# Kernel tuning notes

Hardware: AMD Instinct MI355X
Metric: run time of the kernel (lower is better)

## Reference

```python
import jax, jax.numpy as jnp
import numpy as np

EPS = 1e-5
K_SIZE, STRIDE, DILATION, N_HEADS = 8, 2, 2, 8


def ln2d(x, w, b):
    # LayerNorm2d: normalize over channel axis of NCHW
    m = x.mean(1, keepdims=True)
    v = x.var(1, keepdims=True)
    return (x - m) * jax.lax.rsqrt(v + EPS) * w[None, :, None, None] + b[None, :, None, None]


def setup_inputs() -> dict:
    key = jax.random.key(0)
    ks = jax.random.split(key, 8)
    B, C, H, W = 1, 64, 128, 128
    hid = 2 * C  # ffn_ratio = 2
    f = lambda k, s: jax.random.normal(k, s, jnp.float32) * 0.02
    return dict(
        x=jax.random.normal(ks[0], (B, C, H, W), jnp.float32),
        norm1_w=jnp.ones(C, jnp.float32), norm1_b=jnp.zeros(C, jnp.float32),
        qkv_w=f(ks[1], (3 * C, C)), qkv_b=jnp.zeros(3 * C, jnp.float32),
        qn_w=jnp.ones(C, jnp.float32), qn_b=jnp.zeros(C, jnp.float32),
        kn_w=jnp.ones(C, jnp.float32), kn_b=jnp.zeros(C, jnp.float32),
        proj_w=f(ks[2], (C, C)), proj_b=jnp.zeros(C, jnp.float32),
        gamma1=jnp.full((C,), 0.1, jnp.float32),
        norm2_w=jnp.ones(C, jnp.float32), norm2_b=jnp.zeros(C, jnp.float32),
        fc1_w=f(ks[3], (hid, C)), fc1_b=jnp.zeros(hid, jnp.float32),
        mn_w=jnp.ones(hid, jnp.float32), mn_b=jnp.zeros(hid, jnp.float32),
        fc2_w=f(ks[4], (C, hid)), fc2_b=jnp.zeros(C, jnp.float32),
        gamma2=jnp.full((C,), 0.1, jnp.float32),
    )


def reference(x, norm1_w, norm1_b, qkv_w, qkv_b, qn_w, qn_b, kn_w, kn_b,
              proj_w, proj_b, gamma1, norm2_w, norm2_b,
              fc1_w, fc1_b, mn_w, mn_b, fc2_w, fc2_b, gamma2):
    B, C, H, W = x.shape
    n = N_HEADS
    hd = C // n
    # strided + dilated neighborhood offsets (includes 0 at center)
    off = (jnp.arange(K_SIZE) * STRIDE - (K_SIZE * STRIDE) // 2) * DILATION

    # ---- neighborhood attention branch ----
    xn = ln2d(x, norm1_w, norm1_b)
    qkv = jnp.einsum('oc,bchw->bohw', qkv_w, xn) + qkv_b[None, :, None, None]
    q, k, v = jnp.split(qkv, 3, axis=1)
    q = ln2d(q, qn_w, qn_b)
    k = ln2d(k, kn_w, kn_b)
    q = q.reshape(B, n, hd, H, W)
    k = k.reshape(B, n, hd, H, W)
    v = v.reshape(B, n, hd, H, W)

    pos_h = jnp.arange(H)[:, None] + off[None, :]            # [H, k]
    vh = (pos_h >= 0) & (pos_h < H)
    ih = jnp.clip(pos_h, 0, H - 1)
    pos_w = jnp.arange(W)[:, None] + off[None, :]            # [W, k]
    vw = (pos_w >= 0) & (pos_w < W)
    iw = jnp.clip(pos_w, 0, W - 1)

    # gather neighborhoods: [B,n,hd,H,kh,W,kw]
    Kg = jnp.take(jnp.take(k, ih, axis=3), iw, axis=5)
    Vg = jnp.take(jnp.take(v, ih, axis=3), iw, axis=5)

    scores = jnp.einsum('bnchw,bnchiwj->bnhwij', q, Kg) * (hd ** -0.5)
    mask = vh[:, None, :, None] & vw[None, :, None, :]        # [H,W,kh,kw]
    scores = jnp.where(mask[None, None], scores, -jnp.inf)
    a = jax.nn.softmax(scores.reshape(B, n, H, W, -1), axis=-1).reshape(scores.shape)
    o = jnp.einsum('bnhwij,bnchiwj->bnchw', a, Vg).reshape(B, C, H, W)
    o = jnp.einsum('oc,bchw->bohw', proj_w, o) + proj_b[None, :, None, None]
    x = x + gamma1[None, :, None, None] * o                  # ls1 + residual (drop_path=0)

    # ---- ConvMlp branch: 1x1 conv -> norm -> silu -> 1x1 conv ----
    y = ln2d(x, norm2_w, norm2_b)
    h1 = jnp.einsum('oc,bchw->bohw', fc1_w, y) + fc1_b[None, :, None, None]
    h1 = jax.nn.silu(ln2d(h1, mn_w, mn_b))
    h2 = jnp.einsum('oc,bchw->bohw', fc2_w, h1) + fc2_b[None, :, None, None]
    return x + gamma2[None, :, None, None] * h2
```

## Files before the change

### kernel.cpp

```cpp
#include <hip/hip_runtime.h>
#include <math.h>

#define HW 16384
#define CC 64
#define HID 128
#define EPSV 1e-5f
#define ROW 36
#define SROW 69
#define HDSTR 131072


__global__ __launch_bounds__(256) void k_ln_qkv(
    const float* __restrict__ x,
    const float* __restrict__ n1w, const float* __restrict__ n1b,
    const float* __restrict__ qkvw, const float* __restrict__ qkvb,
    const float* __restrict__ qnw, const float* __restrict__ qnb,
    const float* __restrict__ knw, const float* __restrict__ knb,
    float* __restrict__ qo, float* __restrict__ ko, float* __restrict__ vo)
{
    __shared__ __align__(16) float xs[CC][ROW];
    __shared__ __align__(16) float qk[32][SROW];
    __shared__ __align__(16) float mu1[32], rs1[32], mu2[32], rs2[32];

    const int t = threadIdx.x;
    const int pix0 = blockIdx.x * 32;
    const int sel = blockIdx.y;

    {
        const int c = t >> 2, pxq = (t & 3) * 8;
        *(float4*)&xs[c][pxq]     = *(const float4*)(x + c * HW + pix0 + pxq);
        *(float4*)&xs[c][pxq + 4] = *(const float4*)(x + c * HW + pix0 + pxq + 4);
    }
    __syncthreads();

    if (t < 128) {
        const int px = ((t >> 6) << 4) + (t & 15);
        const int part = (t & 63) >> 4;
        float s = 0.f, ss = 0.f;
        #pragma unroll
        for (int i = 0; i < 16; ++i) { float v = xs[part * 16 + i][px]; s += v; ss += v * v; }
        s += __shfl_xor(s, 16); ss += __shfl_xor(ss, 16);
        s += __shfl_xor(s, 32); ss += __shfl_xor(ss, 32);
        if (part == 0) {
            float m = s * (1.f / CC);
            mu1[px] = m;
            rs1[px] = rsqrtf(ss * (1.f / CC) - m * m + EPSV);
        }
    }
    __syncthreads();

    {
        const int c = t >> 2, pxq = (t & 3) * 8;
        const float wgt = n1w[c], bia = n1b[c];
        #pragma unroll
        for (int hh = 0; hh < 2; ++hh) {
            float4 v = *(float4*)&xs[c][pxq + hh * 4];
            float4 m4 = *(float4*)&mu1[pxq + hh * 4];
            float4 r4 = *(float4*)&rs1[pxq + hh * 4];
            v.x = (v.x - m4.x) * r4.x * wgt + bia;
            v.y = (v.y - m4.y) * r4.y * wgt + bia;
            v.z = (v.z - m4.z) * r4.z * wgt + bia;
            v.w = (v.w - m4.w) * r4.w * wgt + bia;
            *(float4*)&xs[c][pxq + hh * 4] = v;
        }
    }
    __syncthreads();

    {
        const int o0 = (t >> 3) * 2;
        const int px0 = (t & 7) * 4;
        const int ow = sel * 64 + o0;
        float a[2][4];
        #pragma unroll
        for (int j = 0; j < 2; ++j) {
            float b = qkvb[ow + j];
            a[j][0] = b; a[j][1] = b; a[j][2] = b; a[j][3] = b;
        }
        for (int c = 0; c < CC; c += 4) {
            float4 xv[4];
            #pragma unroll
            for (int i = 0; i < 4; ++i) xv[i] = *(float4*)&xs[c + i][px0];
            #pragma unroll
            for (int j = 0; j < 2; ++j) {
                float4 wv = *(const float4*)(qkvw + (ow + j) * CC + c);
                #pragma unroll
                for (int pp = 0; pp < 4; ++pp) {
                    a[j][pp] += wv.x * (&xv[0].x)[pp] + wv.y * (&xv[1].x)[pp]
                              + wv.z * (&xv[2].x)[pp] + wv.w * (&xv[3].x)[pp];
                }
            }
        }
        #pragma unroll
        for (int j = 0; j < 2; ++j) {
            #pragma unroll
            for (int pp = 0; pp < 4; ++pp) qk[px0 + pp][o0 + j] = a[j][pp];
        }
    }
    __syncthreads();

    if (sel < 2) {
        if (t < 128) {
            const int px = ((t >> 6) << 4) + (t & 15);
            const int part = (t & 63) >> 4;
            float s = 0.f, ss = 0.f;
            #pragma unroll
            for (int i = 0; i < 16; ++i) { float v = qk[px][part * 16 + i]; s += v; ss += v * v; }
            s += __shfl_xor(s, 16); ss += __shfl_xor(ss, 16);
            s += __shfl_xor(s, 32); ss += __shfl_xor(ss, 32);
            if (part == 0) {
                float m = s * (1.f / CC);
                mu2[px] = m;
                rs2[px] = rsqrtf(ss * (1.f / CC) - m * m + EPSV);
            }
        }
        __syncthreads();
    }

    const float* lw = (sel == 0) ? qnw : knw;
    const float* lb = (sel == 0) ? qnb : knb;
    float* dst = (sel == 0) ? qo : ((sel == 1) ? ko : vo);
    #pragma unroll
    for (int pass = 0; pass < 2; ++pass) {
        const int px = (t >> 4) + pass * 16;
        const int cg = t & 15;
        const int c = cg * 4;
        const int hd = cg >> 1;
        const int d4 = (cg & 1) * 4;
        const int pixel = pix0 + px;
        const int h = pixel >> 7, w = pixel & 127;
        const int pos = ((h >> 2) * 32 + (w >> 2)) * 16 + (h & 3) * 4 + (w & 3);
        const int gbase = hd * HDSTR + pos * 8 + d4;

        float4 vv = *(float4*)&qk[px][c];
        if (sel < 2) {
            const float mm = mu2[px], rr = rs2[px];
            float4 w4 = *(const float4*)(lw + c);
            float4 b4 = *(const float4*)(lb + c);
            vv.x = (vv.x - mm) * rr * w4.x + b4.x;
            vv.y = (vv.y - mm) * rr * w4.y + b4.y;
            vv.z = (vv.z - mm) * rr * w4.z + b4.z;
            vv.w = (vv.w - mm) * rr * w4.w + b4.w;
        }
        *(float4*)(dst + gbase) = vv;
    }
}

__global__ __launch_bounds__(256) void k_attn(
    const float* __restrict__ q, const float* __restrict__ k, const float* __restrict__ v,
    float* __restrict__ o)
{
    __shared__ __align__(16) float kt[4][15][33][2];
    __shared__ __align__(16) float vt[4][15][33][2];

    const int t = threadIdx.x;
    const int band = blockIdx.x;
    const int sub  = blockIdx.y;
    const int head = blockIdx.z;
    const int hs0 = band * 8;

    const float* kb = k + head * HDSTR;
    const float* vb = v + head * HDSTR;

    for (int idx = t; idx < 960; idx += 256) {
        const int row = idx >> 6;
        const int rem = idx & 63;
        const int ws = rem >> 1;
        const int dh = rem & 1;
        int gr = hs0 - 4 + row;
        gr = gr < 0 ? 0 : (gr > 31 ? 31 : gr);
        const int gaddr = ((gr * 32 + ws) * 16 + sub) * 8 + dh * 4;
        const float4 kv4 = *(const float4*)(kb + gaddr);
        const float4 vv4 = *(const float4*)(vb + gaddr);
        const int dp = dh * 2;
        kt[dp][row][ws][0] = kv4.x;     kt[dp][row][ws][1] = kv4.y;
        kt[dp + 1][row][ws][0] = kv4.z; kt[dp + 1][row][ws][1] = kv4.w;
        vt[dp][row][ws][0] = vv4.x;     vt[dp][row][ws][1] = vv4.y;
        vt[dp + 1][row][ws][0] = vv4.z; vt[dp + 1][row][ws][1] = vv4.w;
    }

    const int r = t >> 5;
    const int ws = t & 31;
    const int hs = hs0 + r;

    const float* qp = q + head * HDSTR + ((hs * 32 + ws) * 16 + sub) * 8;
    const float4 q0 = *(const float4*)qp;
    const float4 q1 = *(const float4*)(qp + 4);
    const float scale = 0.35355339059327373f;

    __syncthreads();

    float s[64];
    float mx0 = -1e30f, mx1 = -1e30f, mx2 = -1e30f, mx3 = -1e30f;
    #pragma unroll
    for (int i = 0; i < 8; ++i) {
        const int lr = r + i;
        const bool vh = (unsigned)(hs + i - 4) < 32u;
        #pragma unroll
        for (int j = 0; j < 8; ++j) {
            const int cs = ws + j - 4;
            const bool valid = vh && ((unsigned)cs < 32u);
            const int cc = cs < 0 ? 0 : (cs > 31 ? 31 : cs);
            const float2 kA = *(const float2*)&kt[0][lr][cc][0];
            const float2 kB = *(const float2*)&kt[1][lr][cc][0];
            const float2 kC = *(const float2*)&kt[2][lr][cc][0];
            const float2 kD = *(const float2*)&kt[3][lr][cc][0];
            float sv = q0.x * kA.x + q0.y * kA.y + q0.z * kB.x + q0.w * kB.y
                     + q1.x * kC.x + q1.y * kC.y + q1.z * kD.x + q1.w * kD.y;
            sv *= scale;
            sv = valid ? sv : -INFINITY;
            s[i * 8 + j] = sv;
            if ((j & 3) == 0)      mx0 = fmaxf(mx0, sv);
            else if ((j & 3) == 1) mx1 = fmaxf(mx1, sv);
            else if ((j & 3) == 2) mx2 = fmaxf(mx2, sv);
            else                   mx3 = fmaxf(mx3, sv);
        }
    }
    const float mx = fmaxf(fmaxf(mx0, mx1), fmaxf(mx2, mx3));

    float l = 0.f;
    float a0 = 0.f, a1 = 0.f, a2 = 0.f, a3 = 0.f, a4 = 0.f, a5 = 0.f, a6 = 0.f, a7 = 0.f;
    #pragma unroll
    for (int i = 0; i < 8; ++i) {
        const int lr = r + i;
        #pragma unroll
        for (int j = 0; j < 8; ++j) {
            const int cs = ws + j - 4;
            const int cc = cs < 0 ? 0 : (cs > 31 ? 31 : cs);
            const float p = __expf(s[i * 8 + j] - mx);
            const float2 vA = *(const float2*)&vt[0][lr][cc][0];
            const float2 vB = *(const float2*)&vt[1][lr][cc][0];
            const float2 vC = *(const float2*)&vt[2][lr][cc][0];
            const float2 vD = *(const float2*)&vt[3][lr][cc][0];
            l += p;
            a0 += p * vA.x;  a1 += p * vA.y;
            a2 += p * vB.x;  a3 += p * vB.y;
            a4 += p * vC.x;  a5 += p * vC.y;
            a6 += p * vD.x;  a7 += p * vD.y;
        }
    }

    const float inv = 1.f / l;
    const int a = sub >> 2, b = sub & 3;
    const int h = hs * 4 + a, w = ws * 4 + b;
    float* op = o + (h * 128 + w) * 64 + head * 8;
    float4 r0 = {a0 * inv, a1 * inv, a2 * inv, a3 * inv};
    float4 r1 = {a4 * inv, a5 * inv, a6 * inv, a7 * inv};
    *(float4*)op = r0;
    *(float4*)(op + 4) = r1;
}

__global__ __launch_bounds__(256) void k_mlp(
    const float* __restrict__ x, const float* __restrict__ oatt,
    const float* __restrict__ pw, const float* __restrict__ pb,
    const float* __restrict__ g1,
    const float* __restrict__ n2w, const float* __restrict__ n2b,
    const float* __restrict__ f1w, const float* __restrict__ f1b,
    const float* __restrict__ mnw, const float* __restrict__ mnb,
    const float* __restrict__ f2w, const float* __restrict__ f2b,
    const float* __restrict__ g2,
    float* __restrict__ out)
{
    __shared__ __align__(16) float xres[CC][ROW];
    __shared__ __align__(16) float tb[CC][ROW];
    __shared__ __align__(16) float h1[HID][ROW];
    __shared__ __align__(16) float mu[32], rs[32];

    const int t = threadIdx.x;
    const int pix0 = blockIdx.x * 32;

    {
        const int c = t >> 2, pxq = (t & 3) * 8;
        *(float4*)&xres[c][pxq]     = *(const float4*)(x + c * HW + pix0 + pxq);
        *(float4*)&xres[c][pxq + 4] = *(const float4*)(x + c * HW + pix0 + pxq + 4);
    }
    #pragma unroll
    for (int pass = 0; pass < 2; ++pass) {
        const int px = (t >> 4) + pass * 16, cg = (t & 15) * 4;
        float4 ov = *(const float4*)(oatt + (pix0 + px) * CC + cg);
        tb[cg][px] = ov.x; tb[cg + 1][px] = ov.y; tb[cg + 2][px] = ov.z; tb[cg + 3][px] = ov.w;
    }
    __syncthreads();

    {
        const int o0 = (t >> 3) * 2;
        const int px0 = (t & 7) * 4;
        float a[2][4];
        #pragma unroll
        for (int j = 0; j < 2; ++j) {
            float b = pb[o0 + j];
            a[j][0] = b; a[j][1] = b; a[j][2] = b; a[j][3] = b;
        }
        for (int c = 0; c < CC; c += 4) {
            float4 xv[4];
            #pragma unroll
            for (int i = 0; i < 4; ++i) xv[i] = *(float4*)&tb[c + i][px0];
            #pragma unroll
            for (int j = 0; j < 2; ++j) {
                float4 wv = *(const float4*)(pw + (o0 + j) * CC + c);
                #pragma unroll
                for (int pp = 0; pp < 4; ++pp) {
                    a[j][pp] += wv.x * (&xv[0].x)[pp] + wv.y * (&xv[1].x)[pp]
                              + wv.z * (&xv[2].x)[pp] + wv.w * (&xv[3].x)[pp];
                }
            }
        }
        #pragma unroll
        for (int j = 0; j < 2; ++j) {
            const float gg = g1[o0 + j];
            #pragma unroll
            for (int pp = 0; pp < 4; ++pp) xres[o0 + j][px0 + pp] += gg * a[j][pp];
        }
    }
    __syncthreads();

    if (t < 128) {
        const int px = ((t >> 6) << 4) + (t & 15);
        const int part = (t & 63) >> 4;
        float s = 0.f, ss = 0.f;
        #pragma unroll
        for (int i = 0; i < 16; ++i) { float v = xres[part * 16 + i][px]; s += v; ss += v * v; }
        s += __shfl_xor(s, 16); ss += __shfl_xor(ss, 16);
        s += __shfl_xor(s, 32); ss += __shfl_xor(ss, 32);
        if (part == 0) {
            float m = s * (1.f / CC);
            mu[px] = m;
            rs[px] = rsqrtf(ss * (1.f / CC) - m * m + EPSV);
        }
    }
    __syncthreads();

    {
        const int c = t >> 2, pxq = (t & 3) * 8;
        const float wgt = n2w[c], bia = n2b[c];
        #pragma unroll
        for (int hh = 0; hh < 2; ++hh) {
            float4 v = *(float4*)&xres[c][pxq + hh * 4];
            float4 m4 = *(float4*)&mu[pxq + hh * 4];
            float4 r4 = *(float4*)&rs[pxq + hh * 4];
            v.x = (v.x - m4.x) * r4.x * wgt + bia;
            v.y = (v.y - m4.y) * r4.y * wgt + bia;
            v.z = (v.z - m4.z) * r4.z * wgt + bia;
            v.w = (v.w - m4.w) * r4.w * wgt + bia;
            *(float4*)&tb[c][pxq + hh * 4] = v;
        }
    }
    __syncthreads();

    {
        const int o0 = (t >> 3) * 4;
        const int px0 = (t & 7) * 4;
        float a[4][4];
        #pragma unroll
        for (int j = 0; j < 4; ++j) {
            float b = f1b[o0 + j];
            a[j][0] = b; a[j][1] = b; a[j][2] = b; a[j][3] = b;
        }
        for (int c = 0; c < CC; c += 4) {
            float4 xv[4];
            #pragma unroll
            for (int i = 0; i < 4; ++i) xv[i] = *(float4*)&tb[c + i][px0];
            #pragma unroll
            for (int j = 0; j < 4; ++j) {
                float4 wv = *(const float4*)(f1w + (o0 + j) * CC + c);
                #pragma unroll
                for (int pp = 0; pp < 4; ++pp) {
                    a[j][pp] += wv.x * (&xv[0].x)[pp] + wv.y * (&xv[1].x)[pp]
                              + wv.z * (&xv[2].x)[pp] + wv.w * (&xv[3].x)[pp];
                }
            }
        }
        #pragma unroll
        for (int j = 0; j < 4; ++j) {
            #pragma unroll
            for (int pp = 0; pp < 4; ++pp) h1[o0 + j][px0 + pp] = a[j][pp];
        }
    }
    __syncthreads();

    if (t < 128) {
        const int px = ((t >> 6) << 4) + (t & 15);
        const int part = (t & 63) >> 4;
        float s = 0.f, ss = 0.f;
        #pragma unroll
        for (int i = 0; i < 32; ++i) { float v = h1[part * 32 + i][px]; s += v; ss += v * v; }
        s += __shfl_xor(s, 16); ss += __shfl_xor(ss, 16);
        s += __shfl_xor(s, 32); ss += __shfl_xor(ss, 32);
        if (part == 0) {
            float m = s * (1.f / HID);
            mu[px] = m;
            rs[px] = rsqrtf(ss * (1.f / HID) - m * m + EPSV);
        }
    }
    __syncthreads();

    {
        const int c = t >> 1, ph = (t & 1) * 16;
        const float wgt = mnw[c], bia = mnb[c];
        #pragma unroll
        for (int qq = 0; qq < 4; ++qq) {
            float4 v = *(float4*)&h1[c][ph + qq * 4];
            float4 m4 = *(float4*)&mu[ph + qq * 4];
            float4 r4 = *(float4*)&rs[ph + qq * 4];
            float hv;
            hv = (v.x - m4.x) * r4.x * wgt + bia; v.x = hv / (1.f + __expf(-hv));
            hv = (v.y - m4.y) * r4.y * wgt + bia; v.y = hv / (1.f + __expf(-hv));
            hv = (v.z - m4.z) * r4.z * wgt + bia; v.z = hv / (1.f + __expf(-hv));
            hv = (v.w - m4.w) * r4.w * wgt + bia; v.w = hv / (1.f + __expf(-hv));
            *(float4*)&h1[c][ph + qq * 4] = v;
        }
    }
    __syncthreads();

    {
        const int o0 = (t >> 3) * 2;
        const int px0 = (t & 7) * 4;
        float a[2][4];
        #pragma unroll
        for (int j = 0; j < 2; ++j) {
            float b = f2b[o0 + j];
            a[j][0] = b; a[j][1] = b; a[j][2] = b; a[j][3] = b;
        }
        for (int c = 0; c < HID; c += 4) {
            float4 xv[4];
            #pragma unroll
            for (int i = 0; i < 4; ++i) xv[i] = *(float4*)&h1[c + i][px0];
            #pragma unroll
            for (int j = 0; j < 2; ++j) {
                float4 wv = *(const float4*)(f2w + (o0 + j) * HID + c);
                #pragma unroll
                for (int pp = 0; pp < 4; ++pp) {
                    a[j][pp] += wv.x * (&xv[0].x)[pp] + wv.y * (&xv[1].x)[pp]
                              + wv.z * (&xv[2].x)[pp] + wv.w * (&xv[3].x)[pp];
                }
            }
        }
        #pragma unroll
        for (int j = 0; j < 2; ++j) {
            const float gg = g2[o0 + j];
            float4 xr = *(float4*)&xres[o0 + j][px0];
            float4 ov = {xr.x + gg * a[j][0], xr.y + gg * a[j][1],
                         xr.z + gg * a[j][2], xr.w + gg * a[j][3]};
            *(float4*)(out + (o0 + j) * HW + pix0 + px0) = ov;
        }
    }
}

extern "C" void kernel_launch(void* const* d_in, const int* in_sizes, int n_in,
                              void* d_out, int out_size, void* d_ws, size_t ws_size,
                              hipStream_t stream) {
    (void)in_sizes; (void)n_in; (void)out_size; (void)ws_size;
    const float* x      = (const float*)d_in[0];
    const float* n1w    = (const float*)d_in[1];
    const float* n1b    = (const float*)d_in[2];
    const float* qkvw   = (const float*)d_in[3];
    const float* qkvb   = (const float*)d_in[4];
    const float* qnw    = (const float*)d_in[5];
    const float* qnb    = (const float*)d_in[6];
    const float* knw    = (const float*)d_in[7];
    const float* knb    = (const float*)d_in[8];
    const float* pw     = (const float*)d_in[9];
    const float* pb     = (const float*)d_in[10];
    const float* g1     = (const float*)d_in[11];
    const float* n2w    = (const float*)d_in[12];
    const float* n2b    = (const float*)d_in[13];
    const float* f1w    = (const float*)d_in[14];
    const float* f1b    = (const float*)d_in[15];
    const float* mnw    = (const float*)d_in[16];
    const float* mnb    = (const float*)d_in[17];
    const float* f2w    = (const float*)d_in[18];
    const float* f2b    = (const float*)d_in[19];
    const float* g2     = (const float*)d_in[20];
    float* out = (float*)d_out;

    float* ws = (float*)d_ws;
    const size_t CHW = (size_t)CC * HW;
    float* qo   = ws;
    float* ko   = ws + CHW;
    float* vo   = ws + 2 * CHW;
    float* oatt = ws + 3 * CHW;

    k_ln_qkv<<<dim3(HW / 32, 3), dim3(256), 0, stream>>>(
        x, n1w, n1b, qkvw, qkvb, qnw, qnb, knw, knb, qo, ko, vo);
    k_attn<<<dim3(4, 16, 8), dim3(256), 0, stream>>>(qo, ko, vo, oatt);
    k_mlp<<<dim3(HW / 32), dim3(256), 0, stream>>>(
        x, oatt, pw, pb, g1, n2w, n2b, f1w, f1b, mnw, mnb, f2w, f2b, g2, out);
}
```

Before: 144.4 us.

## Run MLP-stage 1x1 convs on bf16 MFMA with weights pre-converted in attention kernel

```diff
diff --git a/kernel.cpp b/kernel.cpp
--- a/kernel.cpp
+++ b/kernel.cpp
@@ -8,6 +8,18 @@
 #define ROW 36
 #define SROW 69
 #define HDSTR 131072
+
+typedef __attribute__((ext_vector_type(8))) short bf16x8;
+typedef __attribute__((ext_vector_type(4))) float f32x4v;
+
+__device__ __forceinline__ unsigned short f2bf(float f) {
+    unsigned u = __float_as_uint(f);
+    u += 0x7FFFu + ((u >> 16) & 1u);
+    return (unsigned short)(u >> 16);
+}
+__device__ __forceinline__ unsigned pack2bf(float a, float b) {
+    return (unsigned)f2bf(a) | ((unsigned)f2bf(b) << 16);
+}
 
 
 __global__ __launch_bounds__(256) void k_ln_qkv(
@@ -147,7 +159,10 @@
 
 __global__ __launch_bounds__(256) void k_attn(
     const float* __restrict__ q, const float* __restrict__ k, const float* __restrict__ v,
-    float* __restrict__ o)
+    float* __restrict__ o,
+    const float* __restrict__ pw, const float* __restrict__ f1w, const float* __restrict__ f2w,
+    unsigned short* __restrict__ pwh, unsigned short* __restrict__ f1h,
+    unsigned short* __restrict__ f2h)
 {
     __shared__ __align__(16) float kt[4][15][33][2];
     __shared__ __align__(16) float vt[4][15][33][2];
@@ -158,31 +173,38 @@
     const int head = blockIdx.z;
     const int hs0 = band * 8;
 
+    {
+        const int gtid = ((blockIdx.z * 16 + blockIdx.y) * 4 + blockIdx.x) * 256 + t;
+        if (gtid < 4096)        pwh[gtid] = f2bf(pw[gtid]);
+        else if (gtid < 12288)  f1h[gtid - 4096] = f2bf(f1w[gtid - 4096]);
+        else if (gtid < 20480)  f2h[gtid - 12288] = f2bf(f2w[gtid - 12288]);
+    }
+
     const float* kb = k + head * HDSTR;
     const float* vb = v + head * HDSTR;
 
     for (int idx = t; idx < 960; idx += 256) {
         const int row = idx >> 6;
         const int rem = idx & 63;
-        const int ws = rem >> 1;
+        const int wsc = rem >> 1;
         const int dh = rem & 1;
         int gr = hs0 - 4 + row;
         gr = gr < 0 ? 0 : (gr > 31 ? 31 : gr);
-        const int gaddr = ((gr * 32 + ws) * 16 + sub) * 8 + dh * 4;
+        const int gaddr = ((gr * 32 + wsc) * 16 + sub) * 8 + dh * 4;
         const float4 kv4 = *(const float4*)(kb + gaddr);
         const float4 vv4 = *(const float4*)(vb + gaddr);
         const int dp = dh * 2;
-        kt[dp][row][ws][0] = kv4.x;     kt[dp][row][ws][1] = kv4.y;
-        kt[dp + 1][row][ws][0] = kv4.z; kt[dp + 1][row][ws][1] = kv4.w;
-        vt[dp][row][ws][0] = vv4.x;     vt[dp][row][ws][1] = vv4.y;
-        vt[dp + 1][row][ws][0] = vv4.z; vt[dp + 1][row][ws][1] = vv4.w;
+        kt[dp][row][wsc][0] = kv4.x;     kt[dp][row][wsc][1] = kv4.y;
+        kt[dp + 1][row][wsc][0] = kv4.z; kt[dp + 1][row][wsc][1] = kv4.w;
+        vt[dp][row][wsc][0] = vv4.x;     vt[dp][row][wsc][1] = vv4.y;
+        vt[dp + 1][row][wsc][0] = vv4.z; vt[dp + 1][row][wsc][1] = vv4.w;
     }
 
     const int r = t >> 5;
-    const int ws = t & 31;
+    const int wsc = t & 31;
     const int hs = hs0 + r;
 
-    const float* qp = q + head * HDSTR + ((hs * 32 + ws) * 16 + sub) * 8;
+    const float* qp = q + head * HDSTR + ((hs * 32 + wsc) * 16 + sub) * 8;
     const float4 q0 = *(const float4*)qp;
     const float4 q1 = *(const float4*)(qp + 4);
     const float scale = 0.35355339059327373f;
@@ -197,7 +219,7 @@
         const bool vh = (unsigned)(hs + i - 4) < 32u;
         #pragma unroll
         for (int j = 0; j < 8; ++j) {
-            const int cs = ws + j - 4;
+            const int cs = wsc + j - 4;
             const bool valid = vh && ((unsigned)cs < 32u);
             const int cc = cs < 0 ? 0 : (cs > 31 ? 31 : cs);
             const float2 kA = *(const float2*)&kt[0][lr][cc][0];
@@ -224,7 +246,7 @@
         const int lr = r + i;
         #pragma unroll
         for (int j = 0; j < 8; ++j) {
-            const int cs = ws + j - 4;
+            const int cs = wsc + j - 4;
             const int cc = cs < 0 ? 0 : (cs > 31 ? 31 : cs);
             const float p = __expf(s[i * 8 + j] - mx);
             const float2 vA = *(const float2*)&vt[0][lr][cc][0];
@@ -241,7 +263,7 @@
 
     const float inv = 1.f / l;
     const int a = sub >> 2, b = sub & 3;
-    const int h = hs * 4 + a, w = ws * 4 + b;
+    const int h = hs * 4 + a, w = wsc * 4 + b;
     float* op = o + (h * 128 + w) * 64 + head * 8;
     float4 r0 = {a0 * inv, a1 * inv, a2 * inv, a3 * inv};
     float4 r1 = {a4 * inv, a5 * inv, a6 * inv, a7 * inv};
@@ -251,22 +273,28 @@
 
 __global__ __launch_bounds__(256) void k_mlp(
     const float* __restrict__ x, const float* __restrict__ oatt,
-    const float* __restrict__ pw, const float* __restrict__ pb,
+    const unsigned short* __restrict__ pwh, const float* __restrict__ pb,
     const float* __restrict__ g1,
     const float* __restrict__ n2w, const float* __restrict__ n2b,
-    const float* __restrict__ f1w, const float* __restrict__ f1b,
+    const unsigned short* __restrict__ f1h, const float* __restrict__ f1b,
     const float* __restrict__ mnw, const float* __restrict__ mnb,
-    const float* __restrict__ f2w, const float* __restrict__ f2b,
+    const unsigned short* __restrict__ f2h, const float* __restrict__ f2b,
     const float* __restrict__ g2,
     float* __restrict__ out)
 {
     __shared__ __align__(16) float xres[CC][ROW];
-    __shared__ __align__(16) float tb[CC][ROW];
+    __shared__ __align__(16) unsigned short oh[32][72];
+    __shared__ __align__(16) unsigned short tbh[32][72];
     __shared__ __align__(16) float h1[HID][ROW];
+    __shared__ __align__(16) unsigned short h1h[32][136];
     __shared__ __align__(16) float mu[32], rs[32];
 
     const int t = threadIdx.x;
     const int pix0 = blockIdx.x * 32;
+    const int wv = t >> 6;
+    const int l = t & 63;
+    const int ln = l & 15;
+    const int kg = l >> 4;
 
     {
         const int c = t >> 2, pxq = (t & 3) * 8;
@@ -277,38 +305,31 @@
     for (int pass = 0; pass < 2; ++pass) {
         const int px = (t >> 4) + pass * 16, cg = (t & 15) * 4;
         float4 ov = *(const float4*)(oatt + (pix0 + px) * CC + cg);
-        tb[cg][px] = ov.x; tb[cg + 1][px] = ov.y; tb[cg + 2][px] = ov.z; tb[cg + 3][px] = ov.w;
-    }
-    __syncthreads();
-
-    {
-        const int o0 = (t >> 3) * 2;
-        const int px0 = (t & 7) * 4;
-        float a[2][4];
-        #pragma unroll
-        for (int j = 0; j < 2; ++j) {
-            float b = pb[o0 + j];
-            a[j][0] = b; a[j][1] = b; a[j][2] = b; a[j][3] = b;
-        }
-        for (int c = 0; c < CC; c += 4) {
-            float4 xv[4];
-            #pragma unroll
-            for (int i = 0; i < 4; ++i) xv[i] = *(float4*)&tb[c + i][px0];
-            #pragma unroll
-            for (int j = 0; j < 2; ++j) {
-                float4 wv = *(const float4*)(pw + (o0 + j) * CC + c);
-                #pragma unroll
-                for (int pp = 0; pp < 4; ++pp) {
-                    a[j][pp] += wv.x * (&xv[0].x)[pp] + wv.y * (&xv[1].x)[pp]
-                              + wv.z * (&xv[2].x)[pp] + wv.w * (&xv[3].x)[pp];
-                }
-            }
-        }
-        #pragma unroll
-        for (int j = 0; j < 2; ++j) {
-            const float gg = g1[o0 + j];
-            #pragma unroll
-            for (int pp = 0; pp < 4; ++pp) xres[o0 + j][px0 + pp] += gg * a[j][pp];
+        *(unsigned*)&oh[px][cg]     = pack2bf(ov.x, ov.y);
+        *(unsigned*)&oh[px][cg + 2] = pack2bf(ov.z, ov.w);
+    }
+    __syncthreads();
+
+    {
+        f32x4v acc0 = {0.f, 0.f, 0.f, 0.f}, acc1 = {0.f, 0.f, 0.f, 0.f};
+        const int m = wv * 16 + ln;
+        #pragma unroll
+        for (int kk = 0; kk < 64; kk += 32) {
+            const int k0 = kk + kg * 8;
+            bf16x8 av = *(const bf16x8*)(pwh + m * 64 + k0);
+            bf16x8 b0 = *(const bf16x8*)&oh[ln][k0];
+            bf16x8 b1 = *(const bf16x8*)&oh[16 + ln][k0];
+            acc0 = __builtin_amdgcn_mfma_f32_16x16x32_bf16(av, b0, acc0, 0, 0, 0);
+            acc1 = __builtin_amdgcn_mfma_f32_16x16x32_bf16(av, b1, acc1, 0, 0, 0);
+        }
+        const int r0 = wv * 16 + kg * 4;
+        float4 pb4 = *(const float4*)(pb + r0);
+        float4 g14 = *(const float4*)(g1 + r0);
+        #pragma unroll
+        for (int reg = 0; reg < 4; ++reg) {
+            const int row = r0 + reg;
+            xres[row][ln]      += (&g14.x)[reg] * (acc0[reg] + (&pb4.x)[reg]);
+            xres[row][16 + ln] += (&g14.x)[reg] * (acc1[reg] + (&pb4.x)[reg]);
         }
     }
     __syncthreads();
@@ -330,49 +351,47 @@
     __syncthreads();
 
     {
-        const int c = t >> 2, pxq = (t & 3) * 8;
-        const float wgt = n2w[c], bia = n2b[c];
-        #pragma unroll
-        for (int hh = 0; hh < 2; ++hh) {
-            float4 v = *(float4*)&xres[c][pxq + hh * 4];
-            float4 m4 = *(float4*)&mu[pxq + hh * 4];
-            float4 r4 = *(float4*)&rs[pxq + hh * 4];
-            v.x = (v.x - m4.x) * r4.x * wgt + bia;
-            v.y = (v.y - m4.y) * r4.y * wgt + bia;
-            v.z = (v.z - m4.z) * r4.z * wgt + bia;
-            v.w = (v.w - m4.w) * r4.w * wgt + bia;
-            *(float4*)&tb[c][pxq + hh * 4] = v;
-        }
-    }
-    __syncthreads();
-
-    {
-        const int o0 = (t >> 3) * 4;
-        const int px0 = (t & 7) * 4;
-        float a[4][4];
-        #pragma unroll
-        for (int j = 0; j < 4; ++j) {
-            float b = f1b[o0 + j];
-            a[j][0] = b; a[j][1] = b; a[j][2] = b; a[j][3] = b;
-        }
-        for (int c = 0; c < CC; c += 4) {
-            float4 xv[4];
-            #pragma unroll
-            for (int i = 0; i < 4; ++i) xv[i] = *(float4*)&tb[c + i][px0];
-            #pragma unroll
-            for (int j = 0; j < 4; ++j) {
-                float4 wv = *(const float4*)(f1w + (o0 + j) * CC + c);
-                #pragma unroll
-                for (int pp = 0; pp < 4; ++pp) {
-                    a[j][pp] += wv.x * (&xv[0].x)[pp] + wv.y * (&xv[1].x)[pp]
-                              + wv.z * (&xv[2].x)[pp] + wv.w * (&xv[3].x)[pp];
-                }
-            }
-        }
-        #pragma unroll
-        for (int j = 0; j < 4; ++j) {
-            #pragma unroll
-            for (int pp = 0; pp < 4; ++pp) h1[o0 + j][px0 + pp] = a[j][pp];
+        const int c2 = (t & 31) * 2, px0 = (t >> 5) * 4;
+        const float w0 = n2w[c2], b0 = n2b[c2];
+        const float w1 = n2w[c2 + 1], b1 = n2b[c2 + 1];
+        float4 va = *(float4*)&xres[c2][px0];
+        float4 vb = *(float4*)&xres[c2 + 1][px0];
+        float4 m4 = *(float4*)&mu[px0];
+        float4 r4 = *(float4*)&rs[px0];
+        #pragma unroll
+        for (int i = 0; i < 4; ++i) {
+            float f0 = ((&va.x)[i] - (&m4.x)[i]) * (&r4.x)[i] * w0 + b0;
+            float f1 = ((&vb.x)[i] - (&m4.x)[i]) * (&r4.x)[i] * w1 + b1;
+            *(unsigned*)&tbh[px0 + i][c2] = pack2bf(f0, f1);
+        }
+    }
+    __syncthreads();
+
+    {
+        f32x4v a00 = {0.f,0.f,0.f,0.f}, a01 = {0.f,0.f,0.f,0.f};
+        f32x4v a10 = {0.f,0.f,0.f,0.f}, a11 = {0.f,0.f,0.f,0.f};
+        const int m0 = wv * 32 + ln;
+        #pragma unroll
+        for (int kk = 0; kk < 64; kk += 32) {
+            const int k0 = kk + kg * 8;
+            bf16x8 av0 = *(const bf16x8*)(f1h + m0 * 64 + k0);
+            bf16x8 av1 = *(const bf16x8*)(f1h + (m0 + 16) * 64 + k0);
+            bf16x8 b0 = *(const bf16x8*)&tbh[ln][k0];
+            bf16x8 b1 = *(const bf16x8*)&tbh[16 + ln][k0];
+            a00 = __builtin_amdgcn_mfma_f32_16x16x32_bf16(av0, b0, a00, 0, 0, 0);
+            a01 = __builtin_amdgcn_mfma_f32_16x16x32_bf16(av0, b1, a01, 0, 0, 0);
+            a10 = __builtin_amdgcn_mfma_f32_16x16x32_bf16(av1, b0, a10, 0, 0, 0);
+            a11 = __builtin_amdgcn_mfma_f32_16x16x32_bf16(av1, b1, a11, 0, 0, 0);
+        }
+        const int r0 = wv * 32 + kg * 4;
+        float4 fb0 = *(const float4*)(f1b + r0);
+        float4 fb1 = *(const float4*)(f1b + r0 + 16);
+        #pragma unroll
+        for (int reg = 0; reg < 4; ++reg) {
+            h1[r0 + reg][ln]           = a00[reg] + (&fb0.x)[reg];
+            h1[r0 + reg][16 + ln]      = a01[reg] + (&fb0.x)[reg];
+            h1[r0 + 16 + reg][ln]      = a10[reg] + (&fb1.x)[reg];
+            h1[r0 + 16 + reg][16 + ln] = a11[reg] + (&fb1.x)[reg];
         }
     }
     __syncthreads();
@@ -394,53 +413,49 @@
     __syncthreads();
 
     {
-        const int c = t >> 1, ph = (t & 1) * 16;
-        const float wgt = mnw[c], bia = mnb[c];
-        #pragma unroll
-        for (int qq = 0; qq < 4; ++qq) {
-            float4 v = *(float4*)&h1[c][ph + qq * 4];
-            float4 m4 = *(float4*)&mu[ph + qq * 4];
-            float4 r4 = *(float4*)&rs[ph + qq * 4];
-            float hv;
-            hv = (v.x - m4.x) * r4.x * wgt + bia; v.x = hv / (1.f + __expf(-hv));
-            hv = (v.y - m4.y) * r4.y * wgt + bia; v.y = hv / (1.f + __expf(-hv));
-            hv = (v.z - m4.z) * r4.z * wgt + bia; v.z = hv / (1.f + __expf(-hv));
-            hv = (v.w - m4.w) * r4.w * wgt + bia; v.w = hv / (1.f + __expf(-hv));
-            *(float4*)&h1[c][ph + qq * 4] = v;
-        }
-    }
-    __syncthreads();
-
-    {
-        const int o0 = (t >> 3) * 2;
-        const int px0 = (t & 7) * 4;
-        float a[2][4];
-        #pragma unroll
-        for (int j = 0; j < 2; ++j) {
-            float b = f2b[o0 + j];
-            a[j][0] = b; a[j][1] = b; a[j][2] = b; a[j][3] = b;
-        }
-        for (int c = 0; c < HID; c += 4) {
-            float4 xv[4];
+        const int c2 = (t & 63) * 2, pxm = (t >> 6) * 8;
+        const float w0 = mnw[c2], b0 = mnb[c2];
+        const float w1 = mnw[c2 + 1], b1 = mnb[c2 + 1];
+        #pragma unroll
+        for (int qq = 0; qq < 2; ++qq) {
+            float4 va = *(float4*)&h1[c2][pxm + qq * 4];
+            float4 vb = *(float4*)&h1[c2 + 1][pxm + qq * 4];
+            float4 m4 = *(float4*)&mu[pxm + qq * 4];
+            float4 r4 = *(float4*)&rs[pxm + qq * 4];
             #pragma unroll
-            for (int i = 0; i < 4; ++i) xv[i] = *(float4*)&h1[c + i][px0];
-            #pragma unroll
-            for (int j = 0; j < 2; ++j) {
-                float4 wv = *(const float4*)(f2w + (o0 + j) * HID + c);
-                #pragma unroll
-                for (int pp = 0; pp < 4; ++pp) {
-                    a[j][pp] += wv.x * (&xv[0].x)[pp] + wv.y * (&xv[1].x)[pp]
-                              + wv.z * (&xv[2].x)[pp] + wv.w * (&xv[3].x)[pp];
-                }
+            for (int i = 0; i < 4; ++i) {
+                float h0 = ((&va.x)[i] - (&m4.x)[i]) * (&r4.x)[i] * w0 + b0;
+                float h1v = ((&vb.x)[i] - (&m4.x)[i]) * (&r4.x)[i] * w1 + b1;
+                h0 = h0 / (1.f + __expf(-h0));
+                h1v = h1v / (1.f + __expf(-h1v));
+                *(unsigned*)&h1h[pxm + qq * 4 + i][c2] = pack2bf(h0, h1v);
             }
         }
-        #pragma unroll
-        for (int j = 0; j < 2; ++j) {
-            const float gg = g2[o0 + j];
-            float4 xr = *(float4*)&xres[o0 + j][px0];
-            float4 ov = {xr.x + gg * a[j][0], xr.y + gg * a[j][1],
-                         xr.z + gg * a[j][2], xr.w + gg * a[j][3]};
-            *(float4*)(out + (o0 + j) * HW + pix0 + px0) = ov;
+    }
+    __syncthreads();
+
+    {
+        f32x4v acc0 = {0.f, 0.f, 0.f, 0.f}, acc1 = {0.f, 0.f, 0.f, 0.f};
+        const int m = wv * 16 + ln;
+        #pragma unroll
+        for (int kk = 0; kk < 128; kk += 32) {
+            const int k0 = kk + kg * 8;
+            bf16x8 av = *(const bf16x8*)(f2h + m * 128 + k0);
+            bf16x8 b0 = *(const bf16x8*)&h1h[ln][k0];
+            bf16x8 b1 = *(const bf16x8*)&h1h[16 + ln][k0];
+            acc0 = __builtin_amdgcn_mfma_f32_16x16x32_bf16(av, b0, acc0, 0, 0, 0);
+            acc1 = __builtin_amdgcn_mfma_f32_16x16x32_bf16(av, b1, acc1, 0, 0, 0);
+        }
+        const int r0 = wv * 16 + kg * 4;
+        float4 fb4 = *(const float4*)(f2b + r0);
+        float4 g24 = *(const float4*)(g2 + r0);
+        #pragma unroll
+        for (int reg = 0; reg < 4; ++reg) {
+            const int row = r0 + reg;
+            out[row * HW + pix0 + ln]      = xres[row][ln]
+                                           + (&g24.x)[reg] * (acc0[reg] + (&fb4.x)[reg]);
+            out[row * HW + pix0 + 16 + ln] = xres[row][16 + ln]
+                                           + (&g24.x)[reg] * (acc1[reg] + (&fb4.x)[reg]);
         }
     }
 }
@@ -478,10 +493,15 @@
     float* ko   = ws + CHW;
     float* vo   = ws + 2 * CHW;
     float* oatt = ws + 3 * CHW;
+    unsigned short* wsh = (unsigned short*)(ws + 4 * CHW);
+    unsigned short* pwh = wsh;
+    unsigned short* f1h = wsh + 4096;
+    unsigned short* f2h = wsh + 12288;
 
     k_ln_qkv<<<dim3(HW / 32, 3), dim3(256), 0, stream>>>(
         x, n1w, n1b, qkvw, qkvb, qnw, qnb, knw, knb, qo, ko, vo);
-    k_attn<<<dim3(4, 16, 8), dim3(256), 0, stream>>>(qo, ko, vo, oatt);
+    k_attn<<<dim3(4, 16, 8), dim3(256), 0, stream>>>(
+        qo, ko, vo, oatt, pw, f1w, f2w, pwh, f1h, f2h);
     k_mlp<<<dim3(HW / 32), dim3(256), 0, stream>>>(
-        x, oatt, pw, pb, g1, n2w, n2b, f1w, f1b, mnw, mnb, f2w, f2b, g2, out);
+        x, oatt, pwh, pb, g1, n2w, n2b, f1h, f1b, mnw, mnb, f2h, f2b, g2, out);
 }
```

Result: faster. 135.8 us (-5.9%).
